# Kernel tuning notes

Measured on AMD Instinct MI355X. Metric: run time of the kernel, lower is better.

## Reference

```python
import jax, jax.numpy as jnp
import numpy as np

B, N, D, H, P = 4, 512, 256, 8, 3
HD = D // H
EPS = 1e-5

def _ln(x, g, b):
    m = jnp.mean(x, axis=-1, keepdims=True)
    v = jnp.var(x, axis=-1, keepdims=True)
    return (x - m) * jax.lax.rsqrt(v + EPS) * g + b

def setup_inputs() -> dict:
    key = jax.random.key(0)
    ks = jax.random.split(key, 12)
    s = lambda *sh: 1.0 / np.sqrt(sh[0])
    return {
        "x": jax.random.normal(ks[0], (B, N, D), jnp.float32),
        "mask": jax.random.randint(ks[1], (B, N), 0, 2).astype(bool),
        "pair_feat": jax.random.normal(ks[2], (B, N, N, P), jnp.float32),
        "Wqkv": jax.random.normal(ks[3], (D, 3 * D), jnp.float32) * s(D),
        "Wout": jax.random.normal(ks[4], (D, D), jnp.float32) * s(D),
        "bout": jnp.zeros((D,), jnp.float32),
        "Wp1": jax.random.normal(ks[5], (P, D), jnp.float32) * s(P),
        "bp1": jnp.zeros((D,), jnp.float32),
        "Wp2": jax.random.normal(ks[6], (D, H), jnp.float32) * s(D),
        "bp2": jnp.zeros((H,), jnp.float32),
        "Wf1": jax.random.normal(ks[7], (D, 4 * D), jnp.float32) * s(D),
        "bf1": jnp.zeros((4 * D,), jnp.float32),
        "Wf2": jax.random.normal(ks[8], (4 * D, D), jnp.float32) * s(4 * D),
        "bf2": jnp.zeros((D,), jnp.float32),
        "g1": jnp.ones((D,), jnp.float32), "b1": jnp.zeros((D,), jnp.float32),
        "g2": jnp.ones((D,), jnp.float32), "b2": jnp.zeros((D,), jnp.float32),
    }

def reference(x, mask, pair_feat, Wqkv, Wout, bout, Wp1, bp1, Wp2, bp2,
              Wf1, bf1, Wf2, bf2, g1, b1, g2, b2):
    b_, n_, d_ = x.shape
    scale = HD ** -0.5
    qkv = x @ Wqkv                                  # [B,N,3D]
    q, k, v = jnp.split(qkv, 3, axis=-1)
    q = q.reshape(b_, n_, H, HD)
    k = k.reshape(b_, n_, H, HD)
    v = v.reshape(b_, n_, H, HD)
    logits = jnp.einsum('bihd,bjhd->bhij', q, k) * scale
    # pairwise bias MLP -> per-head bias [B,H,N,N]
    bias = jax.nn.relu(pair_feat @ Wp1 + bp1) @ Wp2 + bp2   # [B,N,N,H]
    logits = logits + jnp.transpose(bias, (0, 3, 1, 2))
    key_mask = ~mask[:, None, None, :]               # [B,1,1,N]
    logits = jnp.where(key_mask, -1e9, logits)
    attn = jax.nn.softmax(logits, axis=-1)
    out = jnp.einsum('bhij,bjhd->bihd', attn, v).reshape(b_, n_, d_)
    out = out @ Wout + bout
    x = _ln(x + out, g1, b1)
    h = jax.nn.gelu(x @ Wf1 + bf1, approximate=False) @ Wf2 + bf2
    return _ln(x + h, g2, b2)
```

## Files before the change

### kernel.cpp

```cpp
#include <hip/hip_runtime.h>
#include <hip/hip_fp16.h>
#include <math.h>

typedef unsigned short u16;
typedef short s16x8 __attribute__((ext_vector_type(8)));
typedef _Float16 f16x8 __attribute__((ext_vector_type(8)));
typedef float f32x4 __attribute__((ext_vector_type(4)));
typedef unsigned int u32x2 __attribute__((ext_vector_type(2)));

constexpr int CB = 4, CN = 512, CD = 256, CH = 8, CHD = 32;
constexpr float CEPS = 1e-5f;
constexpr int M_ROWS = CB * CN;
constexpr float QSCALE = 0.17677669529663687f;

constexpr size_t O_XB    = 0;
constexpr size_t O_QB    = 1048576;
constexpr size_t O_KB    = 2097152;
constexpr size_t O_VT    = 3145728;
constexpr size_t O_WQKVT = 4194304;
constexpr size_t O_WOUTT = O_WQKVT + 393216;
constexpr size_t O_WF1T  = O_WOUTT + 131072;
constexpr size_t O_WF2T  = O_WF1T + 524288;
constexpr size_t O_WP2T  = O_WF2T + 524288;
constexpr size_t O_PACKED= O_WP2T + 8192;
constexpr size_t O_MASKD = O_PACKED + 4096;
constexpr size_t O_BIAS  = O_MASKD + 8192;
constexpr size_t O_AOUT  = O_BIAS + 16777216;
constexpr size_t O_H1B   = O_AOUT + 1048576;
constexpr size_t O_PRE1  = O_H1B + 4194304;
constexpr size_t O_PRE2  = O_PRE1 + 2097152;

__device__ inline u16 f2b(float f) {
  union { float f; unsigned u; } v{f};
  return (u16)((v.u + 0x7FFFu + ((v.u >> 16) & 1u)) >> 16);
}
__device__ inline float b2f(u16 b) {
  union { unsigned u; float f; } v{(unsigned)b << 16};
  return v.f;
}
__device__ inline f32x4 MFMA(s16x8 a, s16x8 b, f32x4 c) {
  return __builtin_amdgcn_mfma_f32_16x16x32_bf16(a, b, c, 0, 0, 0);
}
__device__ inline f32x4 MFMAH(f16x8 a, f16x8 b, f32x4 c) {
  return __builtin_amdgcn_mfma_f32_16x16x32_f16(a, b, c, 0, 0, 0);
}
__device__ inline unsigned cvtpk(float lo, float hi) {
  unsigned r;
  asm("v_cvt_pk_bf16_f32 %0, %1, %2" : "=v"(r) : "v"(lo), "v"(hi));
  return r;
}
__device__ inline unsigned pkmax0(unsigned a) {
  unsigned d;
  asm("v_pk_max_f16 %0, %1, 0" : "=v"(d) : "v"(a));
  return d;
}

__global__ __launch_bounds__(256) void prep_kernel(
    const float* __restrict__ x, const float* __restrict__ Wqkv,
    const float* __restrict__ Wout, const float* __restrict__ Wf1,
    const float* __restrict__ Wf2, const float* __restrict__ Wp2,
    const float* __restrict__ Wp1, const float* __restrict__ bp1,
    const unsigned char* __restrict__ maskraw,
    u16* __restrict__ xb, u16* __restrict__ wqkvt, u16* __restrict__ woutt,
    u16* __restrict__ wf1t, u16* __restrict__ wf2t, u16* __restrict__ wp2t,
    unsigned* __restrict__ packed, int* __restrict__ maskd) {
  __shared__ int mode_max;
  int blk = blockIdx.x, tid = threadIdx.x;
  if (blk < 256) {
    for (int t = tid; t < 512; t += 256) {
      float4 v = ((const float4*)x)[blk * 512 + t];
      u16 o0 = f2b(v.x), o1 = f2b(v.y), o2 = f2b(v.z), o3 = f2b(v.w);
      u32x2 w; w.x = (unsigned)o0 | ((unsigned)o1 << 16);
      w.y = (unsigned)o2 | ((unsigned)o3 << 16);
      *(u32x2*)(xb + (size_t)(blk * 512 + t) * 4) = w;
    }
  } else if (blk < 352) {
    int o0 = (blk - 256) * 2048;
    for (int t = tid; t < 2048; t += 256) {
      int o = o0 + t, n = o >> 8, k = o & 255;
      wqkvt[o] = f2b(Wqkv[k * 768 + n]);
    }
  } else if (blk < 384) {
    int o0 = (blk - 352) * 2048;
    for (int t = tid; t < 2048; t += 256) {
      int o = o0 + t, n = o >> 8, k = o & 255;
      woutt[o] = f2b(Wout[k * 256 + n]);
    }
  } else if (blk < 512) {
    int o0 = (blk - 384) * 2048;
    for (int t = tid; t < 2048; t += 256) {
      int o = o0 + t, n = o >> 8, k = o & 255;
      wf1t[o] = f2b(Wf1[k * 1024 + n]);
    }
  } else if (blk < 640) {
    int o0 = (blk - 512) * 2048;
    for (int t = tid; t < 2048; t += 256) {
      int o = o0 + t, n = o >> 10, k = o & 1023;
      wf2t[o] = f2b(Wf2[k * 256 + n]);
    }
  } else if (blk == 640) {
    for (int t = tid; t < 4096; t += 256) {
      int h = t >> 8, c = t & 255;
      wp2t[t] = (h < 8) ? __half_as_ushort(__float2half(Wp2[c * 8 + h])) : (u16)0;
    }
    if (tid < 128) {
      int p = tid * 2;
      unsigned w0 = (unsigned)__half_as_ushort(__float2half(Wp1[p]))
                  | ((unsigned)__half_as_ushort(__float2half(Wp1[p + 1])) << 16);
      unsigned w1 = (unsigned)__half_as_ushort(__float2half(Wp1[256 + p]))
                  | ((unsigned)__half_as_ushort(__float2half(Wp1[256 + p + 1])) << 16);
      unsigned w2 = (unsigned)__half_as_ushort(__float2half(Wp1[512 + p]))
                  | ((unsigned)__half_as_ushort(__float2half(Wp1[512 + p + 1])) << 16);
      unsigned bb = (unsigned)__half_as_ushort(__float2half(bp1[p]))
                  | ((unsigned)__half_as_ushort(__float2half(bp1[p + 1])) << 16);
      uint4 o; o.x = w0; o.y = w1; o.z = w2; o.w = bb;
      ((uint4*)packed)[tid] = o;
    }
  } else {
    if (tid == 0) mode_max = 0;
    __syncthreads();
    int lm = 0;
    for (int i = tid; i < CB*CN; i += 256)
      if ((i & 3) != 0) lm = max(lm, (int)maskraw[i]);
    atomicMax(&mode_max, lm);
    __syncthreads();
    int mv = mode_max;
    for (int i = tid; i < CB*CN; i += 256) {
      int val;
      if (mv == 0)      val = (((const int*)maskraw)[i] != 0);
      else if (mv == 1) val = (maskraw[i] != 0);
      else              val = (((const unsigned int*)maskraw)[i] != 0);
      maskd[i] = val;
    }
  }
}

__global__ __launch_bounds__(256) void qkv_pbias_kernel(
    const u16* __restrict__ A, const u16* __restrict__ Wt,
    u16* __restrict__ qb, u16* __restrict__ kb, u16* __restrict__ vt,
    const float* __restrict__ pf, const unsigned* __restrict__ packed,
    const u16* __restrict__ wp2t, const float* __restrict__ bp2,
    u16* __restrict__ biasout) {
  __shared__ uint4 smem[1024];
  const int blk = blockIdx.x, tid = threadIdx.x;
  const int lane = tid & 63, w = tid >> 6;
  if (blk < 384) {
    u16* As = (u16*)smem;
    u16* Bs = (u16*)smem + 64 * 64;
    const int wm = w >> 1, wn = w & 1;
    const int bm = (blk / 12) * 64, bn = (blk % 12) * 64;
    f32x4 fz = {0.f, 0.f, 0.f, 0.f};
    f32x4 acc[2][2] = {{fz, fz}, {fz, fz}};
    for (int k0 = 0; k0 < 256; k0 += 64) {
#pragma unroll
      for (int t = tid; t < 512; t += 256) {
        int r = t >> 3, s = t & 7;
        s16x8 v = *(const s16x8*)(A + (size_t)(bm + r) * 256 + k0 + s * 8);
        *(s16x8*)(As + r * 64 + ((s ^ (r & 7)) << 3)) = v;
      }
#pragma unroll
      for (int t = tid; t < 512; t += 256) {
        int r = t >> 3, s = t & 7;
        s16x8 v = *(const s16x8*)(Wt + (size_t)(bn + r) * 256 + k0 + s * 8);
        *(s16x8*)(Bs + r * 64 + ((s ^ (r & 7)) << 3)) = v;
      }
      __syncthreads();
#pragma unroll
      for (int ks = 0; ks < 2; ++ks) {
        s16x8 af[2], bf[2];
#pragma unroll
        for (int mf = 0; mf < 2; ++mf) {
          int r = wm * 32 + mf * 16 + (lane & 15);
          int s = ks * 4 + (lane >> 4);
          af[mf] = *(const s16x8*)(As + r * 64 + ((s ^ (r & 7)) << 3));
        }
#pragma unroll
        for (int nf = 0; nf < 2; ++nf) {
          int r = wn * 32 + nf * 16 + (lane & 15);
          int s = ks * 4 + (lane >> 4);
          bf[nf] = *(const s16x8*)(Bs + r * 64 + ((s ^ (r & 7)) << 3));
        }
#pragma unroll
        for (int mf = 0; mf < 2; ++mf)
#pragma unroll
          for (int nf = 0; nf < 2; ++nf)
            acc[mf][nf] = MFMA(af[mf], bf[nf], acc[mf][nf]);
      }
      __syncthreads();
    }
#pragma unroll
    for (int mf = 0; mf < 2; ++mf) {
#pragma unroll
      for (int nf = 0; nf < 2; ++nf) {
#pragma unroll
        for (int r = 0; r < 4; ++r) {
          int m = bm + wm * 32 + mf * 16 + (lane >> 4) * 4 + r;
          int n = bn + wn * 32 + nf * 16 + (lane & 15);
          float v = acc[mf][nf][r];
          if (n < 256) {
            qb[(size_t)m * 256 + n] = f2b(v * QSCALE);
          } else if (n < 512) {
            kb[(size_t)m * 256 + (n - 256)] = f2b(v);
          } else {
            int nv = n - 512, h = nv >> 5, d = nv & 31;
            int bb = m >> 9, j = m & 511;
            vt[(size_t)((bb * 8 + h) * 32 + d) * 512 + j] = f2b(v);
          }
        }
      }
    }
  } else {
    uint4* pk = smem;
    float* pfl = (float*)(smem + 128);
    const int bid = blk - 384;
    const int b = bid >> 9, i = bid & 511;
    const int q = lane >> 4, hr = lane & 15;
    if (tid < 128) pk[tid] = ((const uint4*)packed)[tid];
    const float4* pfr = (const float4*)(pf + (size_t)(b * 512 + i) * 1536);
#pragma unroll
    for (int t = tid; t < 384; t += 256) ((float4*)pfl)[t] = pfr[t];
    __syncthreads();
    __half2 f0d[8], f1d[8], f2d[8];
#pragma unroll
    for (int t = 0; t < 8; ++t) {
      int j = w * 128 + t * 16 + hr;
      f0d[t] = __float2half2_rn(pfl[j * 3 + 0]);
      f1d[t] = __float2half2_rn(pfl[j * 3 + 1]);
      f2d[t] = __float2half2_rn(pfl[j * 3 + 2]);
    }
    f32x4 fz = {0.f, 0.f, 0.f, 0.f};
    f32x4 acc[8] = {fz, fz, fz, fz, fz, fz, fz, fz};
    for (int chunk = 0; chunk < 8; ++chunk) {
      f16x8 wfrag = *(const f16x8*)(wp2t + hr * 256 + chunk * 32 + q * 8);
      int pbase = chunk * 16 + q * 4;
      __half2 w0[4], w1[4], w2[4], bb[4];
#pragma unroll
      for (int p = 0; p < 4; ++p) {
        uint4 c = pk[pbase + p];
        w0[p] = *(const __half2*)&c.x;
        w1[p] = *(const __half2*)&c.y;
        w2[p] = *(const __half2*)&c.z;
        bb[p] = *(const __half2*)&c.w;
      }
#pragma unroll
      for (int t = 0; t < 8; ++t) {
        union { unsigned u[4]; f16x8 v; } af;
#pragma unroll
        for (int p = 0; p < 4; ++p) {
          __half2 h = __hfma2(f0d[t], w0[p], bb[p]);
          h = __hfma2(f1d[t], w1[p], h);
          h = __hfma2(f2d[t], w2[p], h);
          af.u[p] = pkmax0(*(const unsigned*)&h);
        }
        acc[t] = MFMAH(af.v, wfrag, acc[t]);
      }
    }
    if (hr < 8) {
      float bb = bp2[hr];
      size_t base = ((size_t)(b * 8 + hr) * 512 + i) * 512;
#pragma unroll
      for (int t = 0; t < 8; ++t) {
        int j0 = w * 128 + t * 16 + q * 4;
        u32x2 o;
        o.x = cvtpk(acc[t][0] + bb, acc[t][1] + bb);
        o.y = cvtpk(acc[t][2] + bb, acc[t][3] + bb);
        *(u32x2*)(biasout + base + j0) = o;
      }
    }
  }
}

__global__ __launch_bounds__(256) void mgemm_res(
    const u16* __restrict__ A, const u16* __restrict__ Wt,
    const float* __restrict__ bias, const float* __restrict__ R,
    float* __restrict__ outf, int N, int K) {
  __shared__ u16 As[32 * 64];
  __shared__ u16 Bs[64 * 64];
  const int tid = threadIdx.x;
  const int lane = tid & 63, w = tid >> 6;
  const int wm = w >> 1, wn = w & 1;
  const int bm = blockIdx.y * 32, bn = blockIdx.x * 64;
  f32x4 fz = {0.f, 0.f, 0.f, 0.f};
  f32x4 acc[2] = {fz, fz};
  for (int k0 = 0; k0 < K; k0 += 64) {
    for (int t = tid; t < 256; t += 256) {
      int r = t >> 3, s = t & 7;
      s16x8 v = *(const s16x8*)(A + (size_t)(bm + r) * K + k0 + s * 8);
      *(s16x8*)(As + r * 64 + ((s ^ (r & 7)) << 3)) = v;
    }
#pragma unroll
    for (int t = tid; t < 512; t += 256) {
      int r = t >> 3, s = t & 7;
      s16x8 v = *(const s16x8*)(Wt + (size_t)(bn + r) * K + k0 + s * 8);
      *(s16x8*)(Bs + r * 64 + ((s ^ (r & 7)) << 3)) = v;
    }
    __syncthreads();
#pragma unroll
    for (int ks = 0; ks < 2; ++ks) {
      int r = wm * 16 + (lane & 15);
      int s = ks * 4 + (lane >> 4);
      s16x8 af = *(const s16x8*)(As + r * 64 + ((s ^ (r & 7)) << 3));
#pragma unroll
      for (int nf = 0; nf < 2; ++nf) {
        int br = wn * 32 + nf * 16 + (lane & 15);
        s16x8 bf = *(const s16x8*)(Bs + br * 64 + ((s ^ (br & 7)) << 3));
        acc[nf] = MFMA(af, bf, acc[nf]);
      }
    }
    __syncthreads();
  }
#pragma unroll
  for (int nf = 0; nf < 2; ++nf) {
#pragma unroll
    for (int r = 0; r < 4; ++r) {
      int m = bm + wm * 16 + (lane >> 4) * 4 + r;
      int n = bn + wn * 32 + nf * 16 + (lane & 15);
      outf[(size_t)m * N + n] = acc[nf][r] + bias[n] + R[(size_t)m * N + n];
    }
  }
}

__global__ __launch_bounds__(256) void ffn1_kernel(
    const float* __restrict__ pre1, const u16* __restrict__ Wt,
    const float* __restrict__ bias, const float* __restrict__ g1,
    const float* __restrict__ b1, u16* __restrict__ outb) {
  __shared__ u16 As[64 * 64];
  __shared__ u16 Bs[64 * 64];
  __shared__ float rowm[64], rowr[64];
  const int tid = threadIdx.x;
  const int lane = tid & 63, w = tid >> 6;
  const int wm = w >> 1, wn = w & 1;
  const int bm = blockIdx.y * 64, bn = blockIdx.x * 64;
  {
    int r = tid >> 2, qd = tid & 3;
    const float4* pr = (const float4*)(pre1 + (size_t)(bm + r) * 256 + qd * 64);
    float s = 0.f, ss = 0.f;
#pragma unroll
    for (int u = 0; u < 16; ++u) {
      float4 v = pr[u];
      s += v.x + v.y + v.z + v.w;
      ss += v.x*v.x + v.y*v.y + v.z*v.z + v.w*v.w;
    }
    s += __shfl_xor(s, 1); ss += __shfl_xor(ss, 1);
    s += __shfl_xor(s, 2); ss += __shfl_xor(ss, 2);
    if (qd == 0) {
      float mean = s * (1.0f / 256.0f);
      float var  = ss * (1.0f / 256.0f) - mean * mean;
      rowm[r] = mean; rowr[r] = rsqrtf(var + CEPS);
    }
  }
  __syncthreads();
  f32x4 fz = {0.f, 0.f, 0.f, 0.f};
  f32x4 acc[2][2] = {{fz, fz}, {fz, fz}};
  for (int k0 = 0; k0 < 256; k0 += 64) {
#pragma unroll
    for (int t = tid; t < 512; t += 256) {
      int r = t >> 3, s = t & 7;
      float mean = rowm[r], rstd = rowr[r];
      const float4* pr = (const float4*)(pre1 + (size_t)(bm + r) * 256 + k0 + s * 8);
      float4 a0 = pr[0], a1 = pr[1];
      const float4* gp = (const float4*)(g1 + k0 + s * 8);
      const float4* bp = (const float4*)(b1 + k0 + s * 8);
      float4 g0 = gp[0], g1v = gp[1], c0 = bp[0], c1 = bp[1];
      union { unsigned u[4]; s16x8 v; } pk2;
      pk2.u[0] = cvtpk((a0.x-mean)*rstd*g0.x + c0.x, (a0.y-mean)*rstd*g0.y + c0.y);
      pk2.u[1] = cvtpk((a0.z-mean)*rstd*g0.z + c0.z, (a0.w-mean)*rstd*g0.w + c0.w);
      pk2.u[2] = cvtpk((a1.x-mean)*rstd*g1v.x + c1.x, (a1.y-mean)*rstd*g1v.y + c1.y);
      pk2.u[3] = cvtpk((a1.z-mean)*rstd*g1v.z + c1.z, (a1.w-mean)*rstd*g1v.w + c1.w);
      *(s16x8*)(As + r * 64 + ((s ^ (r & 7)) << 3)) = pk2.v;
    }
#pragma unroll
    for (int t = tid; t < 512; t += 256) {
      int r = t >> 3, s = t & 7;
      s16x8 v = *(const s16x8*)(Wt + (size_t)(bn + r) * 256 + k0 + s * 8);
      *(s16x8*)(Bs + r * 64 + ((s ^ (r & 7)) << 3)) = v;
    }
    __syncthreads();
#pragma unroll
    for (int ks = 0; ks < 2; ++ks) {
      s16x8 af[2], bf[2];
#pragma unroll
      for (int mf = 0; mf < 2; ++mf) {
        int r = wm * 32 + mf * 16 + (lane & 15);
        int s = ks * 4 + (lane >> 4);
        af[mf] = *(const s16x8*)(As + r * 64 + ((s ^ (r & 7)) << 3));
      }
#pragma unroll
      for (int nf = 0; nf < 2; ++nf) {
        int r = wn * 32 + nf * 16 + (lane & 15);
        int s = ks * 4 + (lane >> 4);
        bf[nf] = *(const s16x8*)(Bs + r * 64 + ((s ^ (r & 7)) << 3));
      }
#pragma unroll
      for (int mf = 0; mf < 2; ++mf)
#pragma unroll
        for (int nf = 0; nf < 2; ++nf)
          acc[mf][nf] = MFMA(af[mf], bf[nf], acc[mf][nf]);
    }
    __syncthreads();
  }
#pragma unroll
  for (int mf = 0; mf < 2; ++mf) {
#pragma unroll
    for (int nf = 0; nf < 2; ++nf) {
#pragma unroll
      for (int r = 0; r < 4; ++r) {
        int m = bm + wm * 32 + mf * 16 + (lane >> 4) * 4 + r;
        int n = bn + wn * 32 + nf * 16 + (lane & 15);
        float gv = acc[mf][nf][r] + bias[n];
        gv = 0.5f * gv * (1.0f + erff(gv * 0.70710678118654752f));
        outb[(size_t)m * 1024 + n] = f2b(gv);
      }
    }
  }
}

__global__ __launch_bounds__(256) void ffn2_kernel(
    const u16* __restrict__ A, const u16* __restrict__ Wt,
    const float* __restrict__ bias, const float* __restrict__ pre1,
    const float* __restrict__ g1, const float* __restrict__ b1,
    float* __restrict__ outf) {
  __shared__ u16 As[32 * 64];
  __shared__ u16 Bs[64 * 64];
  __shared__ float rowm[32], rowr[32];
  const int tid = threadIdx.x;
  const int lane = tid & 63, w = tid >> 6;
  const int wm = w >> 1, wn = w & 1;
  const int bm = blockIdx.y * 32, bn = blockIdx.x * 64;
  {
    int r = tid >> 3, od = tid & 7;
    const float4* pr = (const float4*)(pre1 + (size_t)(bm + r) * 256 + od * 32);
    float s = 0.f, ss = 0.f;
#pragma unroll
    for (int u = 0; u < 8; ++u) {
      float4 v = pr[u];
      s += v.x + v.y + v.z + v.w;
      ss += v.x*v.x + v.y*v.y + v.z*v.z + v.w*v.w;
    }
    s += __shfl_xor(s, 1); ss += __shfl_xor(ss, 1);
    s += __shfl_xor(s, 2); ss += __shfl_xor(ss, 2);
    s += __shfl_xor(s, 4); ss += __shfl_xor(ss, 4);
    if (od == 0) {
      float mean = s * (1.0f / 256.0f);
      float var  = ss * (1.0f / 256.0f) - mean * mean;
      rowm[r] = mean; rowr[r] = rsqrtf(var + CEPS);
    }
  }
  __syncthreads();
  f32x4 fz = {0.f, 0.f, 0.f, 0.f};
  f32x4 acc[2] = {fz, fz};
  for (int k0 = 0; k0 < 1024; k0 += 64) {
    for (int t = tid; t < 256; t += 256) {
      int r = t >> 3, s = t & 7;
      s16x8 v = *(const s16x8*)(A + (size_t)(bm + r) * 1024 + k0 + s * 8);
      *(s16x8*)(As + r * 64 + ((s ^ (r & 7)) << 3)) = v;
    }
#pragma unroll
    for (int t = tid; t < 512; t += 256) {
      int r = t >> 3, s = t & 7;
      s16x8 v = *(const s16x8*)(Wt + (size_t)(bn + r) * 1024 + k0 + s * 8);
      *(s16x8*)(Bs + r * 64 + ((s ^ (r & 7)) << 3)) = v;
    }
    __syncthreads();
#pragma unroll
    for (int ks = 0; ks < 2; ++ks) {
      int r = wm * 16 + (lane & 15);
      int s = ks * 4 + (lane >> 4);
      s16x8 af = *(const s16x8*)(As + r * 64 + ((s ^ (r & 7)) << 3));
#pragma unroll
      for (int nf = 0; nf < 2; ++nf) {
        int br = wn * 32 + nf * 16 + (lane & 15);
        s16x8 bf = *(const s16x8*)(Bs + br * 64 + ((s ^ (br & 7)) << 3));
        acc[nf] = MFMA(af, bf, acc[nf]);
      }
    }
    __syncthreads();
  }
#pragma unroll
  for (int nf = 0; nf < 2; ++nf) {
#pragma unroll
    for (int r = 0; r < 4; ++r) {
      int m = bm + wm * 16 + (lane >> 4) * 4 + r;
      int n = bn + wn * 32 + nf * 16 + (lane & 15);
      float mean = rowm[m - bm], rstd = rowr[m - bm];
      float xr = (pre1[(size_t)m * 256 + n] - mean) * rstd * g1[n] + b1[n];
      outf[(size_t)m * 256 + n] = acc[nf][r] + bias[n] + xr;
    }
  }
}

__global__ __launch_bounds__(512) void flash_kernel(
    const u16* __restrict__ qb, const u16* __restrict__ kb,
    const u16* __restrict__ vt, const u16* __restrict__ biasin,
    const int* __restrict__ maskd, u16* __restrict__ aout) {
  const int i0 = blockIdx.x * 64, h = blockIdx.y, b = blockIdx.z;
  const int tid = threadIdx.x;
  const int lane = tid & 63, w = tid >> 6;
  const int mf = w & 3, jhalf = w >> 2;
  __shared__ u16 qs[64 * 32];
  __shared__ u16 ksh[128 * 32];
  __shared__ u16 vs[32 * 128];
  __shared__ u16 ps[8][16 * 64];
  __shared__ float cmb[4][2][16][2];
  for (int t = tid; t < 256; t += 512) {
    int r = t >> 2, s = t & 3;
    s16x8 v = *(const s16x8*)(qb + (size_t)(b * 512 + i0 + r) * 256 + h * 32 + s * 8);
    *(s16x8*)(qs + r * 32 + ((s ^ (r & 3)) << 3)) = v;
  }
  f32x4 fz = {0.f, 0.f, 0.f, 0.f};
  f32x4 oacc[2] = {fz, fz};
  float mrun[4] = {-3e38f, -3e38f, -3e38f, -3e38f};
  float lrun[4] = {0.f, 0.f, 0.f, 0.f};
  const int* mrow = maskd + b * 512;
  const int jj0 = jhalf * 64;
  const int il = mf * 16 + (lane >> 4) * 4;
  const u16* bbase = biasin + ((size_t)((b * 8 + h) * 512 + i0 + il)) * 512
                   + jj0 + (lane & 15);
  for (int jc = 0; jc < 4; ++jc) {
    int j0 = jc * 128;
    for (int t = tid; t < 512; t += 512) {
      int r = t >> 2, s = t & 3;
      s16x8 v = *(const s16x8*)(kb + (size_t)(b * 512 + j0 + r) * 256 + h * 32 + s * 8);
      *(s16x8*)(ksh + r * 32 + ((s ^ (r & 3)) << 3)) = v;
    }
    for (int t = tid; t < 512; t += 512) {
      int r = t >> 4, s = t & 15;
      s16x8 v = *(const s16x8*)(vt + (size_t)((b * 8 + h) * 32 + r) * 512 + j0 + s * 8);
      *(s16x8*)(vs + r * 128 + (((s & 8) | ((s & 7) ^ (r & 7))) << 3)) = v;
    }
    u16 bvr[4][4];
#pragma unroll
    for (int jf = 0; jf < 4; ++jf)
#pragma unroll
      for (int r = 0; r < 4; ++r)
        bvr[jf][r] = bbase[(size_t)r * 512 + j0 + jf * 16];
    __syncthreads();
    int mk[4];
#pragma unroll
    for (int jf = 0; jf < 4; ++jf)
      mk[jf] = mrow[j0 + jj0 + jf * 16 + (lane & 15)];
    int arow = mf * 16 + (lane & 15);
    s16x8 af = *(const s16x8*)(qs + arow * 32 + (((lane >> 4) ^ (arow & 3)) << 3));
    f32x4 sm[4];
#pragma unroll
    for (int jf = 0; jf < 4; ++jf) {
      int brow = jj0 + jf * 16 + (lane & 15);
      s16x8 bfr = *(const s16x8*)(ksh + brow * 32 + (((lane >> 4) ^ (brow & 3)) << 3));
      sm[jf] = MFMA(af, bfr, fz);
    }
#pragma unroll
    for (int jf = 0; jf < 4; ++jf) {
#pragma unroll
      for (int r = 0; r < 4; ++r) {
        float sval = sm[jf][r] + b2f(bvr[jf][r]);
        sm[jf][r] = mk[jf] ? sval : -1e9f;
      }
    }
    float mx[4];
#pragma unroll
    for (int r = 0; r < 4; ++r)
      mx[r] = fmaxf(fmaxf(sm[0][r], sm[1][r]), fmaxf(sm[2][r], sm[3][r]));
#pragma unroll
    for (int d = 1; d < 16; d <<= 1)
#pragma unroll
      for (int r = 0; r < 4; ++r) mx[r] = fmaxf(mx[r], __shfl_xor(mx[r], d));
    float psl[4] = {0.f, 0.f, 0.f, 0.f};
#pragma unroll
    for (int jf = 0; jf < 4; ++jf)
#pragma unroll
      for (int r = 0; r < 4; ++r) {
        float p = __expf(sm[jf][r] - mx[r]);
        sm[jf][r] = p; psl[r] += p;
      }
#pragma unroll
    for (int d = 1; d < 16; d <<= 1)
#pragma unroll
      for (int r = 0; r < 4; ++r) psl[r] += __shfl_xor(psl[r], d);
    if ((lane & 15) == 0) {
#pragma unroll
      for (int r = 0; r < 4; ++r) {
        int row = (lane >> 4) * 4 + r;
        cmb[mf][jhalf][row][0] = mx[r];
        cmb[mf][jhalf][row][1] = psl[r];
      }
    }
    __syncthreads();
    float selfs[4];
#pragma unroll
    for (int r = 0; r < 4; ++r) {
      int row = (lane >> 4) * 4 + r;
      float omx = cmb[mf][1 - jhalf][row][0];
      float ops = cmb[mf][1 - jhalf][row][1];
      float tm = fmaxf(mx[r], omx);
      float nm = fmaxf(mrun[r], tm);
      float sc = __expf(mrun[r] - nm);
      selfs[r] = __expf(mx[r] - nm);
      float ptile = psl[r] * selfs[r] + ops * __expf(omx - nm);
      lrun[r] = lrun[r] * sc + ptile;
      mrun[r] = nm;
      oacc[0][r] *= sc; oacc[1][r] *= sc;
    }
    u16* pw = &ps[w][0];
#pragma unroll
    for (int jf = 0; jf < 4; ++jf) {
      int jcol = jf * 16 + (lane & 15);
      int slot = jcol >> 3, el = jcol & 7;
#pragma unroll
      for (int r = 0; r < 4; ++r) {
        int row = (lane >> 4) * 4 + r;
        pw[row * 64 + ((slot ^ (row & 7)) << 3) + el] = f2b(sm[jf][r] * selfs[r]);
      }
    }
#pragma unroll
    for (int kw = 0; kw < 2; ++kw) {
      int prow = lane & 15;
      s16x8 pa = *(const s16x8*)(pw + prow * 64 + (((kw * 4 + (lane >> 4)) ^ (prow & 7)) << 3));
#pragma unroll
      for (int df = 0; df < 2; ++df) {
        int drow = df * 16 + (lane & 15);
        int jcol = jj0 + kw * 32 + ((lane >> 4) << 3);
        int slot = jcol >> 3;
        s16x8 vb = *(const s16x8*)(vs + drow * 128 + (((slot & 8) | ((slot & 7) ^ (drow & 7))) << 3));
        oacc[df] = MFMA(pa, vb, oacc[df]);
      }
    }
    __syncthreads();
  }
  float* obuf = (float*)&ps[0][0];
  if (jhalf == 1) {
#pragma unroll
    for (int r = 0; r < 4; ++r) {
      int row = mf * 16 + (lane >> 4) * 4 + r;
#pragma unroll
      for (int df = 0; df < 2; ++df)
        obuf[row * 33 + df * 16 + (lane & 15)] = oacc[df][r];
    }
  }
  __syncthreads();
  if (jhalf == 0) {
#pragma unroll
    for (int r = 0; r < 4; ++r) {
      float inv = 1.0f / lrun[r];
      int row = mf * 16 + (lane >> 4) * 4 + r;
      int i = i0 + row;
#pragma unroll
      for (int df = 0; df < 2; ++df) {
        int d = df * 16 + (lane & 15);
        float o = (oacc[df][r] + obuf[row * 33 + d]) * inv;
        aout[(size_t)(b * 512 + i) * 256 + h * 32 + d] = f2b(o);
      }
    }
  }
}

__global__ __launch_bounds__(256) void ln_kernel(
    const float* __restrict__ in, const float* __restrict__ g,
    const float* __restrict__ be, float* __restrict__ op) {
  int row = blockIdx.x * 4 + (threadIdx.x >> 6);
  int lane = threadIdx.x & 63;
  const float* x = in + (size_t)row * CD;
  float4 v = *(const float4*)&x[lane * 4];
  float s  = v.x + v.y + v.z + v.w;
  float ss = v.x*v.x + v.y*v.y + v.z*v.z + v.w*v.w;
#pragma unroll
  for (int off = 32; off > 0; off >>= 1) {
    s  += __shfl_xor(s, off);
    ss += __shfl_xor(ss, off);
  }
  float mean = s * (1.0f / CD);
  float var  = ss * (1.0f / CD) - mean * mean;
  float inv  = rsqrtf(var + CEPS);
  float4 gg = *(const float4*)&g[lane * 4];
  float4 bb = *(const float4*)&be[lane * 4];
  float4 o;
  o.x = (v.x - mean) * inv * gg.x + bb.x;
  o.y = (v.y - mean) * inv * gg.y + bb.y;
  o.z = (v.z - mean) * inv * gg.z + bb.z;
  o.w = (v.w - mean) * inv * gg.w + bb.w;
  *(float4*)&op[(size_t)row * CD + lane * 4] = o;
}

extern "C" void kernel_launch(void* const* d_in, const int* in_sizes, int n_in,
                              void* d_out, int out_size, void* d_ws, size_t ws_size,
                              hipStream_t stream) {
  (void)in_sizes; (void)n_in; (void)out_size; (void)ws_size;
  const float* x    = (const float*)d_in[0];
  const void*  mask = d_in[1];
  const float* pf   = (const float*)d_in[2];
  const float* Wqkv = (const float*)d_in[3];
  const float* Wout = (const float*)d_in[4];
  const float* bout = (const float*)d_in[5];
  const float* Wp1  = (const float*)d_in[6];
  const float* bp1  = (const float*)d_in[7];
  const float* Wp2  = (const float*)d_in[8];
  const float* bp2  = (const float*)d_in[9];
  const float* Wf1  = (const float*)d_in[10];
  const float* bf1  = (const float*)d_in[11];
  const float* Wf2  = (const float*)d_in[12];
  const float* bf2  = (const float*)d_in[13];
  const float* g1   = (const float*)d_in[14];
  const float* b1   = (const float*)d_in[15];
  const float* g2   = (const float*)d_in[16];
  const float* b2   = (const float*)d_in[17];

  char* ws = (char*)d_ws;
  u16* xb     = (u16*)(ws + O_XB);
  u16* qb     = (u16*)(ws + O_QB);
  u16* kb     = (u16*)(ws + O_KB);
  u16* vt     = (u16*)(ws + O_VT);
  u16* wqkvt  = (u16*)(ws + O_WQKVT);
  u16* woutt  = (u16*)(ws + O_WOUTT);
  u16* wf1t   = (u16*)(ws + O_WF1T);
  u16* wf2t   = (u16*)(ws + O_WF2T);
  u16* wp2t   = (u16*)(ws + O_WP2T);
  unsigned* packed = (unsigned*)(ws + O_PACKED);
  int* maskd  = (int*)(ws + O_MASKD);
  u16* biasb  = (u16*)(ws + O_BIAS);
  u16* aout   = (u16*)(ws + O_AOUT);
  u16* h1b    = (u16*)(ws + O_H1B);
  float* pre1 = (float*)(ws + O_PRE1);
  float* pre2 = (float*)(ws + O_PRE2);
  float* out  = (float*)d_out;

  hipLaunchKernelGGL(prep_kernel, dim3(642), dim3(256), 0, stream,
                     x, Wqkv, Wout, Wf1, Wf2, Wp2, Wp1, bp1,
                     (const unsigned char*)mask,
                     xb, wqkvt, woutt, wf1t, wf2t, wp2t, packed, maskd);
  hipLaunchKernelGGL(qkv_pbias_kernel, dim3(2432), dim3(256), 0, stream,
                     xb, wqkvt, qb, kb, vt,
                     pf, packed, wp2t, bp2, biasb);
  hipLaunchKernelGGL(flash_kernel, dim3(8, 8, 4), dim3(512), 0, stream,
                     qb, kb, vt, biasb, maskd, aout);
  hipLaunchKernelGGL(mgemm_res, dim3(4, 64), dim3(256), 0, stream,
                     aout, woutt, bout, x, pre1, 256, 256);
  hipLaunchKernelGGL(ffn1_kernel, dim3(16, 32), dim3(256), 0, stream,
                     pre1, wf1t, bf1, g1, b1, h1b);
  hipLaunchKernelGGL(ffn2_kernel, dim3(4, 64), dim3(256), 0, stream,
                     h1b, wf2t, bf2, pre1, g1, b1, pre2);
  hipLaunchKernelGGL(ln_kernel, dim3(M_ROWS / 4), dim3(256), 0, stream,
                     pre2, g2, b2, out);
}
```

Baseline: 99.99 us.

## Compact unmasked key indices to skip masked pairs in bias MLP and attention

The prep kernel now builds, per batch, a compacted list of unmasked key indices and their count using wave ballots, instead of writing a dense mask. The pair-bias MLP evaluates and stores bias only for compacted keys. The flash kernel gathers K and V rows through the index list and loops only over as many 128-key tiles as there are valid keys, so masked keys are neither read nor computed. V is now stored row-major and transposed element by element into shared memory during the gather, which adds scattered LDS stores. A batch with every key masked would now produce a different result from the reference's uniform softmax.

```diff
diff --git a/kernel.cpp b/kernel.cpp
--- a/kernel.cpp
+++ b/kernel.cpp
@@ -16,19 +16,20 @@
 constexpr size_t O_XB    = 0;
 constexpr size_t O_QB    = 1048576;
 constexpr size_t O_KB    = 2097152;
-constexpr size_t O_VT    = 3145728;
+constexpr size_t O_VB    = 3145728;
 constexpr size_t O_WQKVT = 4194304;
 constexpr size_t O_WOUTT = O_WQKVT + 393216;
 constexpr size_t O_WF1T  = O_WOUTT + 131072;
 constexpr size_t O_WF2T  = O_WF1T + 524288;
 constexpr size_t O_WP2T  = O_WF2T + 524288;
 constexpr size_t O_PACKED= O_WP2T + 8192;
-constexpr size_t O_MASKD = O_PACKED + 4096;
-constexpr size_t O_BIAS  = O_MASKD + 8192;
+constexpr size_t O_JIDX  = O_PACKED + 4096;
+constexpr size_t O_BIAS  = O_JIDX + 8192;
 constexpr size_t O_AOUT  = O_BIAS + 16777216;
 constexpr size_t O_H1B   = O_AOUT + 1048576;
 constexpr size_t O_PRE1  = O_H1B + 4194304;
 constexpr size_t O_PRE2  = O_PRE1 + 2097152;
+constexpr size_t O_CNT   = O_PRE2 + 2097152;
 
 __device__ inline u16 f2b(float f) {
   union { float f; unsigned u; } v{f};
@@ -63,8 +64,10 @@
     const unsigned char* __restrict__ maskraw,
     u16* __restrict__ xb, u16* __restrict__ wqkvt, u16* __restrict__ woutt,
     u16* __restrict__ wf1t, u16* __restrict__ wf2t, u16* __restrict__ wp2t,
-    unsigned* __restrict__ packed, int* __restrict__ maskd) {
+    unsigned* __restrict__ packed, int* __restrict__ jidxg,
+    int* __restrict__ cntg) {
   __shared__ int mode_max;
+  __shared__ int mdec[2048];
   int blk = blockIdx.x, tid = threadIdx.x;
   if (blk < 256) {
     for (int t = tid; t < 512; t += 256) {
@@ -130,17 +133,33 @@
       if (mv == 0)      val = (((const int*)maskraw)[i] != 0);
       else if (mv == 1) val = (maskraw[i] != 0);
       else              val = (((const unsigned int*)maskraw)[i] != 0);
-      maskd[i] = val;
+      mdec[i] = val;
+    }
+    __syncthreads();
+    int w = tid >> 6, lane = tid & 63;
+    if (w < 4) {
+      int b = w, basei = 0;
+      for (int c = 0; c < 8; ++c) {
+        int j = c * 64 + lane;
+        int m = mdec[b * 512 + j];
+        unsigned long long bal = __ballot(m != 0);
+        int off = __popcll(bal & ((1ull << lane) - 1ull));
+        if (m) jidxg[b * 512 + basei + off] = j;
+        basei += (int)__popcll(bal);
+      }
+      if (lane == 0) cntg[b] = basei;
+      for (int p = basei + lane; p < 512; p += 64) jidxg[b * 512 + p] = 0;
     }
   }
 }
 
 __global__ __launch_bounds__(256) void qkv_pbias_kernel(
     const u16* __restrict__ A, const u16* __restrict__ Wt,
-    u16* __restrict__ qb, u16* __restrict__ kb, u16* __restrict__ vt,
+    u16* __restrict__ qb, u16* __restrict__ kb, u16* __restrict__ vb,
     const float* __restrict__ pf, const unsigned* __restrict__ packed,
     const u16* __restrict__ wp2t, const float* __restrict__ bp2,
-    u16* __restrict__ biasout) {
+    const int* __restrict__ jidxg, const int* __restrict__ cntg,
+    u16* __restrict__ biasc) {
   __shared__ uint4 smem[1024];
   const int blk = blockIdx.x, tid = threadIdx.x;
   const int lane = tid & 63, w = tid >> 6;
@@ -202,9 +221,7 @@
           } else if (n < 512) {
             kb[(size_t)m * 256 + (n - 256)] = f2b(v);
           } else {
-            int nv = n - 512, h = nv >> 5, d = nv & 31;
-            int bb = m >> 9, j = m & 511;
-            vt[(size_t)((bb * 8 + h) * 32 + d) * 512 + j] = f2b(v);
+            vb[(size_t)m * 256 + (n - 512)] = f2b(v);
           }
         }
       }
@@ -212,6 +229,7 @@
   } else {
     uint4* pk = smem;
     float* pfl = (float*)(smem + 128);
+    int* ji = (int*)(smem + 512);
     const int bid = blk - 384;
     const int b = bid >> 9, i = bid & 511;
     const int q = lane >> 4, hr = lane & 15;
@@ -219,14 +237,18 @@
     const float4* pfr = (const float4*)(pf + (size_t)(b * 512 + i) * 1536);
 #pragma unroll
     for (int t = tid; t < 384; t += 256) ((float4*)pfl)[t] = pfr[t];
+    for (int t = tid; t < 512; t += 256) ji[t] = jidxg[b * 512 + t];
+    const int cnt = cntg[b];
     __syncthreads();
     __half2 f0d[8], f1d[8], f2d[8];
 #pragma unroll
     for (int t = 0; t < 8; ++t) {
-      int j = w * 128 + t * 16 + hr;
-      f0d[t] = __float2half2_rn(pfl[j * 3 + 0]);
-      f1d[t] = __float2half2_rn(pfl[j * 3 + 1]);
-      f2d[t] = __float2half2_rn(pfl[j * 3 + 2]);
+      if (w * 128 + t * 16 < cnt) {
+        int jsrc = ji[w * 128 + t * 16 + hr];
+        f0d[t] = __float2half2_rn(pfl[jsrc * 3 + 0]);
+        f1d[t] = __float2half2_rn(pfl[jsrc * 3 + 1]);
+        f2d[t] = __float2half2_rn(pfl[jsrc * 3 + 2]);
+      }
     }
     f32x4 fz = {0.f, 0.f, 0.f, 0.f};
     f32x4 acc[8] = {fz, fz, fz, fz, fz, fz, fz, fz};
@@ -244,15 +266,17 @@
       }
 #pragma unroll
       for (int t = 0; t < 8; ++t) {
-        union { unsigned u[4]; f16x8 v; } af;
-#pragma unroll
-        for (int p = 0; p < 4; ++p) {
-          __half2 h = __hfma2(f0d[t], w0[p], bb[p]);
-          h = __hfma2(f1d[t], w1[p], h);
-          h = __hfma2(f2d[t], w2[p], h);
-          af.u[p] = pkmax0(*(const unsigned*)&h);
+        if (w * 128 + t * 16 < cnt) {
+          union { unsigned u[4]; f16x8 v; } af;
+#pragma unroll
+          for (int p = 0; p < 4; ++p) {
+            __half2 h = __hfma2(f0d[t], w0[p], bb[p]);
+            h = __hfma2(f1d[t], w1[p], h);
+            h = __hfma2(f2d[t], w2[p], h);
+            af.u[p] = pkmax0(*(const unsigned*)&h);
+          }
+          acc[t] = MFMAH(af.v, wfrag, acc[t]);
         }
-        acc[t] = MFMAH(af.v, wfrag, acc[t]);
       }
     }
     if (hr < 8) {
@@ -260,11 +284,13 @@
       size_t base = ((size_t)(b * 8 + hr) * 512 + i) * 512;
 #pragma unroll
       for (int t = 0; t < 8; ++t) {
-        int j0 = w * 128 + t * 16 + q * 4;
-        u32x2 o;
-        o.x = cvtpk(acc[t][0] + bb, acc[t][1] + bb);
-        o.y = cvtpk(acc[t][2] + bb, acc[t][3] + bb);
-        *(u32x2*)(biasout + base + j0) = o;
+        if (w * 128 + t * 16 < cnt) {
+          int p0 = w * 128 + t * 16 + q * 4;
+          u32x2 o;
+          o.x = cvtpk(acc[t][0] + bb, acc[t][1] + bb);
+          o.y = cvtpk(acc[t][2] + bb, acc[t][3] + bb);
+          *(u32x2*)(biasc + base + p0) = o;
+        }
       }
     }
   }
@@ -491,8 +517,9 @@
 
 __global__ __launch_bounds__(512) void flash_kernel(
     const u16* __restrict__ qb, const u16* __restrict__ kb,
-    const u16* __restrict__ vt, const u16* __restrict__ biasin,
-    const int* __restrict__ maskd, u16* __restrict__ aout) {
+    const u16* __restrict__ vb, const u16* __restrict__ biasc,
+    const int* __restrict__ jidxg, const int* __restrict__ cntg,
+    u16* __restrict__ aout) {
   const int i0 = blockIdx.x * 64, h = blockIdx.y, b = blockIdx.z;
   const int tid = threadIdx.x;
   const int lane = tid & 63, w = tid >> 6;
@@ -502,31 +529,42 @@
   __shared__ u16 vs[32 * 128];
   __shared__ u16 ps[8][16 * 64];
   __shared__ float cmb[4][2][16][2];
+  __shared__ int ji[512];
+  for (int t = tid; t < 512; t += 512) ji[t] = jidxg[b * 512 + t];
   for (int t = tid; t < 256; t += 512) {
     int r = t >> 2, s = t & 3;
     s16x8 v = *(const s16x8*)(qb + (size_t)(b * 512 + i0 + r) * 256 + h * 32 + s * 8);
     *(s16x8*)(qs + r * 32 + ((s ^ (r & 3)) << 3)) = v;
   }
+  const int cnt = cntg[b];
+  __syncthreads();
   f32x4 fz = {0.f, 0.f, 0.f, 0.f};
   f32x4 oacc[2] = {fz, fz};
   float mrun[4] = {-3e38f, -3e38f, -3e38f, -3e38f};
   float lrun[4] = {0.f, 0.f, 0.f, 0.f};
-  const int* mrow = maskd + b * 512;
   const int jj0 = jhalf * 64;
   const int il = mf * 16 + (lane >> 4) * 4;
-  const u16* bbase = biasin + ((size_t)((b * 8 + h) * 512 + i0 + il)) * 512
+  const u16* bbase = biasc + ((size_t)((b * 8 + h) * 512 + i0 + il)) * 512
                    + jj0 + (lane & 15);
-  for (int jc = 0; jc < 4; ++jc) {
+  const int NJT = (cnt + 127) >> 7;
+  for (int jc = 0; jc < NJT; ++jc) {
     int j0 = jc * 128;
-    for (int t = tid; t < 512; t += 512) {
-      int r = t >> 2, s = t & 3;
-      s16x8 v = *(const s16x8*)(kb + (size_t)(b * 512 + j0 + r) * 256 + h * 32 + s * 8);
+    {
+      int r = tid >> 2, s = tid & 3;
+      int jsrc = ji[j0 + r];
+      s16x8 v = *(const s16x8*)(kb + (size_t)(b * 512 + jsrc) * 256 + h * 32 + s * 8);
       *(s16x8*)(ksh + r * 32 + ((s ^ (r & 3)) << 3)) = v;
     }
-    for (int t = tid; t < 512; t += 512) {
-      int r = t >> 4, s = t & 15;
-      s16x8 v = *(const s16x8*)(vt + (size_t)((b * 8 + h) * 32 + r) * 512 + j0 + s * 8);
-      *(s16x8*)(vs + r * 128 + (((s & 8) | ((s & 7) ^ (r & 7))) << 3)) = v;
+    {
+      int r = tid >> 2, s = tid & 3;
+      int jsrc = ji[j0 + r];
+      s16x8 v = *(const s16x8*)(vb + (size_t)(b * 512 + jsrc) * 256 + h * 32 + s * 8);
+      int slot = r >> 3, el = r & 7;
+#pragma unroll
+      for (int e = 0; e < 8; ++e) {
+        int d = s * 8 + e;
+        vs[d * 128 + (((slot & 8) | ((slot & 7) ^ (d & 7))) << 3) + el] = (u16)v[e];
+      }
     }
     u16 bvr[4][4];
 #pragma unroll
@@ -538,7 +576,7 @@
     int mk[4];
 #pragma unroll
     for (int jf = 0; jf < 4; ++jf)
-      mk[jf] = mrow[j0 + jj0 + jf * 16 + (lane & 15)];
+      mk[jf] = (j0 + jj0 + jf * 16 + (lane & 15)) < cnt;
     int arow = mf * 16 + (lane & 15);
     s16x8 af = *(const s16x8*)(qs + arow * 32 + (((lane >> 4) ^ (arow & 3)) << 3));
     f32x4 sm[4];
@@ -620,8 +658,8 @@
         int drow = df * 16 + (lane & 15);
         int jcol = jj0 + kw * 32 + ((lane >> 4) << 3);
         int slot = jcol >> 3;
-        s16x8 vb = *(const s16x8*)(vs + drow * 128 + (((slot & 8) | ((slot & 7) ^ (drow & 7))) << 3));
-        oacc[df] = MFMA(pa, vb, oacc[df]);
+        s16x8 vv = *(const s16x8*)(vs + drow * 128 + (((slot & 8) | ((slot & 7) ^ (drow & 7))) << 3));
+        oacc[df] = MFMA(pa, vv, oacc[df]);
       }
     }
     __syncthreads();
@@ -707,15 +745,16 @@
   u16* xb     = (u16*)(ws + O_XB);
   u16* qb     = (u16*)(ws + O_QB);
   u16* kb     = (u16*)(ws + O_KB);
-  u16* vt     = (u16*)(ws + O_VT);
+  u16* vb     = (u16*)(ws + O_VB);
   u16* wqkvt  = (u16*)(ws + O_WQKVT);
   u16* woutt  = (u16*)(ws + O_WOUTT);
   u16* wf1t   = (u16*)(ws + O_WF1T);
   u16* wf2t   = (u16*)(ws + O_WF2T);
   u16* wp2t   = (u16*)(ws + O_WP2T);
   unsigned* packed = (unsigned*)(ws + O_PACKED);
-  int* maskd  = (int*)(ws + O_MASKD);
-  u16* biasb  = (u16*)(ws + O_BIAS);
+  int* jidxg  = (int*)(ws + O_JIDX);
+  int* cntg   = (int*)(ws + O_CNT);
+  u16* biasc  = (u16*)(ws + O_BIAS);
   u16* aout   = (u16*)(ws + O_AOUT);
   u16* h1b    = (u16*)(ws + O_H1B);
   float* pre1 = (float*)(ws + O_PRE1);
@@ -725,12 +764,12 @@
   hipLaunchKernelGGL(prep_kernel, dim3(642), dim3(256), 0, stream,
                      x, Wqkv, Wout, Wf1, Wf2, Wp2, Wp1, bp1,
                      (const unsigned char*)mask,
-                     xb, wqkvt, woutt, wf1t, wf2t, wp2t, packed, maskd);
+                     xb, wqkvt, woutt, wf1t, wf2t, wp2t, packed, jidxg, cntg);
   hipLaunchKernelGGL(qkv_pbias_kernel, dim3(2432), dim3(256), 0, stream,
-                     xb, wqkvt, qb, kb, vt,
-                     pf, packed, wp2t, bp2, biasb);
+                     xb, wqkvt, qb, kb, vb,
+                     pf, packed, wp2t, bp2, jidxg, cntg, biasc);
   hipLaunchKernelGGL(flash_kernel, dim3(8, 8, 4), dim3(512), 0, stream,
-                     qb, kb, vt, biasb, maskd, aout);
+                     qb, kb, vb, biasc, jidxg, cntg, aout);
   hipLaunchKernelGGL(mgemm_res, dim3(4, 64), dim3(256), 0, stream,
                      aout, woutt, bout, x, pre1, 256, 256);
   hipLaunchKernelGGL(ffn1_kernel, dim3(16, 32), dim3(256), 0, stream,
```

New measurement: 101.1 us. No clear change (+1.1%).
